# Kernel tuning notes

Hardware: AMD Instinct MI355X
Metric: run time of the kernel (lower is better)

The kernel has to match this reference:

```python
import jax, jax.numpy as jnp
import numpy as np

B, S, D = 1, 2048, 2048
H, HD = 16, 128  # n_heads, head_dim
ROPE_BASE = 100000.0


def setup_inputs() -> dict:
    key = jax.random.key(0)
    k0, k1, k2 = jax.random.split(key, 3)
    x = jax.random.normal(k0, (B, S, D), jnp.float32)
    # real RoPE table: (seq_len, head_dim//2, 2) holding (cos, sin)
    inv_freq = 1.0 / (ROPE_BASE ** (np.arange(0, HD, 2, dtype=np.float64) / HD))
    t = np.arange(S, dtype=np.float64)[:, None] * inv_freq[None, :]
    freqs_cis = jnp.asarray(np.stack([np.cos(t), np.sin(t)], axis=-1), jnp.float32)
    input_pos = jnp.arange(S, dtype=jnp.int32)
    Wqkv = jax.random.normal(k1, (D, 3 * D), jnp.float32) * (D ** -0.5)
    bqkv = jnp.zeros((3 * D,), jnp.float32)
    Wdense = jax.random.normal(k2, (D, D), jnp.float32) * (D ** -0.5)
    bdense = jnp.zeros((D,), jnp.float32)
    return {"x": x, "freqs_cis": freqs_cis, "input_pos": input_pos,
            "Wqkv": Wqkv, "bqkv": bqkv, "Wdense": Wdense, "bdense": bdense}


def apply_rotary_emb(x, freqs_cis):
    # x: [B, S, H, HD]; freqs_cis: [S, HD//2, 2]
    xs = x.reshape(*x.shape[:-1], -1, 2)  # [B,S,H,HD/2,2]
    fc = freqs_cis.reshape(1, xs.shape[1], 1, xs.shape[3], 2)
    out = jnp.stack([
        xs[..., 0] * fc[..., 0] - xs[..., 1] * fc[..., 1],
        xs[..., 1] * fc[..., 0] + xs[..., 0] * fc[..., 1],
    ], axis=-1)
    return out.reshape(x.shape).astype(x.dtype)


def reference(x, freqs_cis, input_pos, Wqkv, bqkv, Wdense, bdense):
    b, s, d = x.shape
    qkv = x @ Wqkv + bqkv                      # fused QKV projection
    q, k, v = jnp.split(qkv, 3, axis=-1)
    q = q.reshape(b, s, H, HD)
    k = k.reshape(b, s, H, HD)
    v = v.reshape(b, s, H, HD)
    q = apply_rotary_emb(q, freqs_cis)
    k = apply_rotary_emb(k, freqs_cis)
    # KV-cache update (cache batch = 1, max_seq = context_length)
    k_cache = jnp.zeros((1, S, H, HD), jnp.float32)
    v_cache = jnp.zeros((1, S, H, HD), jnp.float32)
    k_full = k_cache.at[:, input_pos].set(k)
    v_full = v_cache.at[:, input_pos].set(v)
    # causal SDPA in [B, H, S, HD] layout
    qh = q.transpose(0, 2, 1, 3)
    kh = k_full.transpose(0, 2, 1, 3)
    vh = v_full.transpose(0, 2, 1, 3)
    scale = HD ** -0.5
    scores = jnp.einsum('bhqd,bhkd->bhqk', qh, kh) * scale  # [B,H,S,S]
    causal = jnp.tril(jnp.ones((s, S), dtype=bool))
    scores = jnp.where(causal, scores, jnp.finfo(scores.dtype).min)
    attn = jax.nn.softmax(scores, axis=-1)
    ctx = jnp.einsum('bhqk,bhkd->bhqd', attn, vh)
    ctx = ctx.transpose(0, 2, 1, 3).reshape(b, s, d)
    return ctx @ Wdense + bdense
```

## Files before the change

kernel.cpp:

```cpp
#include <hip/hip_runtime.h>

#define S 2048
#define D 2048
#define H 16
#define HD 128
#define N3 6144

typedef __attribute__((ext_vector_type(8))) _Float16 f16x8;
typedef __attribute__((ext_vector_type(4))) float f32x4;
typedef unsigned short ushort_t;
typedef unsigned int uint_t;

__device__ __forceinline__ ushort_t f16_rne(float f) {
    _Float16 h = (_Float16)f;
    return __builtin_bit_cast(ushort_t, h);
}
__device__ __forceinline__ float f16_f32(ushort_t u) {
    return (float)__builtin_bit_cast(_Float16, u);
}

__global__ __launch_bounds__(256) void convert_f16_kernel(
    const float* __restrict__ in, ushort_t* __restrict__ hi)
{
    const int base = blockIdx.x * 512 + threadIdx.x;
    const float4* in4 = (const float4*)in;
    float4 a = in4[base];
    float4 b = in4[base + 256];
    ((ushort4*)hi)[base] = make_ushort4(f16_rne(a.x), f16_rne(a.y),
                                        f16_rne(a.z), f16_rne(a.w));
    ((ushort4*)hi)[base + 256] = make_ushort4(f16_rne(b.x), f16_rne(b.y),
                                              f16_rne(b.z), f16_rne(b.w));
}

__global__ __launch_bounds__(256) void convert_t_kernel(
    const float* __restrict__ in, ushort_t* __restrict__ hi,
    int Kdim, int Ndim)
{
    __shared__ float tile[32][33];
    const int k0 = blockIdx.x * 32, n0 = blockIdx.y * 32;
    const int row = threadIdx.x >> 3;
    const int c4  = (threadIdx.x & 7) * 4;
    float4 v = *(const float4*)&in[(size_t)(k0 + row) * Ndim + n0 + c4];
    tile[row][c4 + 0] = v.x;
    tile[row][c4 + 1] = v.y;
    tile[row][c4 + 2] = v.z;
    tile[row][c4 + 3] = v.w;
    __syncthreads();
    const int n  = threadIdx.x >> 3;
    const int kc = (threadIdx.x & 7) * 4;
    const float v0 = tile[kc + 0][n], v1 = tile[kc + 1][n];
    const float v2 = tile[kc + 2][n], v3 = tile[kc + 3][n];
    const size_t off = (size_t)(n0 + n) * Kdim + k0 + kc;
    *(ushort4*)&hi[off] = make_ushort4(f16_rne(v0), f16_rne(v1),
                                       f16_rne(v2), f16_rne(v3));
}

__device__ __forceinline__ void gload16(const ushort_t* g, ushort_t* l) {
    __builtin_amdgcn_global_load_lds(
        (const __attribute__((address_space(1))) unsigned int*)g,
        (__attribute__((address_space(3))) unsigned int*)l, 16, 0, 0);
}

__device__ __forceinline__ void vwait4() { asm volatile("s_waitcnt vmcnt(4)" ::: "memory"); }
__device__ __forceinline__ void vwait3() { asm volatile("s_waitcnt vmcnt(3)" ::: "memory"); }
__device__ __forceinline__ void vwait0() { asm volatile("s_waitcnt vmcnt(0)" ::: "memory"); }
__device__ __forceinline__ void lwait0() { asm volatile("s_waitcnt lgkmcnt(0)" ::: "memory"); }

#define QNT 32

__device__ __forceinline__ void mm_core_v4(
    const ushort_t* __restrict__ At, const ushort_t* __restrict__ Bt,
    ushort_t* lds, const int t, f32x4 (&acc)[4][2])
{
    const int w = t >> 6, lane = t & 63;
    const int lr = lane & 15, quad = lane >> 4;
    const int wm = (w >> 2) * 64;
    const int wn = (w & 3) * 32;

    const int srow = w * 8 + (lane >> 3);
    const int schk = ((lane & 7) ^ (lane >> 3)) * 8;
    const int ldsw = w * 512;

    auto stageAB = [&](int Tt) {
        ushort_t* dbase = lds + (Tt & 1) * 16384;
        const size_t koff = (size_t)Tt * 64 + schk;
        gload16(At + (size_t)srow * D + koff,        dbase + ldsw);
        gload16(At + (size_t)(srow + 64) * D + koff, dbase + 4096 + ldsw);
        gload16(Bt + (size_t)srow * D + koff,        dbase + 8192 + ldsw);
        gload16(Bt + (size_t)(srow + 64) * D + koff, dbase + 12288 + ldsw);
    };

    const int aoff = (wm + lr) * 64;
    const int boff = 8192 + (wn + lr) * 64;
    const int sw0 = ((0 * 4 + quad) ^ (lr & 7)) * 8;
    const int sw1 = ((1 * 4 + quad) ^ (lr & 7)) * 8;

    stageAB(0);
    stageAB(1);
    vwait4();
    __builtin_amdgcn_sched_barrier(0);
    __builtin_amdgcn_s_barrier();

    f16x8 a[4], b[2];
    for (int T = 0; T < QNT; T++) {
        const ushort_t* base = lds + (T & 1) * 16384;
        #pragma unroll
        for (int i = 0; i < 4; i++)
            a[i] = *(const f16x8*)&base[aoff + i * 1024 + sw0];
        #pragma unroll
        for (int n = 0; n < 2; n++)
            b[n] = *(const f16x8*)&base[boff + n * 1024 + sw0];
        lwait0();
        __builtin_amdgcn_sched_barrier(0);
        __builtin_amdgcn_s_setprio(1);
        #pragma unroll
        for (int i = 0; i < 4; i++)
            #pragma unroll
            for (int n = 0; n < 2; n++)
                acc[i][n] = __builtin_amdgcn_mfma_f32_16x16x32_f16(
                    a[i], b[n], acc[i][n], 0, 0, 0);
        __builtin_amdgcn_s_setprio(0);
        #pragma unroll
        for (int i = 0; i < 4; i++)
            a[i] = *(const f16x8*)&base[aoff + i * 1024 + sw1];
        #pragma unroll
        for (int n = 0; n < 2; n++)
            b[n] = *(const f16x8*)&base[boff + n * 1024 + sw1];
        lwait0();
        __builtin_amdgcn_sched_barrier(0);
        __builtin_amdgcn_s_barrier();
        if (T < QNT - 2) stageAB(T + 2);
        __builtin_amdgcn_s_setprio(1);
        #pragma unroll
        for (int i = 0; i < 4; i++)
            #pragma unroll
            for (int n = 0; n < 2; n++)
                acc[i][n] = __builtin_amdgcn_mfma_f32_16x16x32_f16(
                    a[i], b[n], acc[i][n], 0, 0, 0);
        __builtin_amdgcn_s_setprio(0);
        if (T < QNT - 2)       vwait4();
        else if (T == QNT - 2) vwait0();
        __builtin_amdgcn_s_barrier();
    }
}

__device__ __forceinline__ void mm_core_v4h(
    const ushort_t* __restrict__ At, const ushort_t* __restrict__ Bt,
    ushort_t* lds, const int t, f32x4 (&acc)[2][2])
{
    const int w = t >> 6, lane = t & 63;
    const int lr = lane & 15, quad = lane >> 4;
    const int wm = (w >> 2) * 32;
    const int wn = (w & 3) * 32;

    const int srow = w * 8 + (lane >> 3);
    const int schk = ((lane & 7) ^ (lane >> 3)) * 8;
    const int ldsw = w * 512;

    auto stageAB = [&](int Tt) {
        ushort_t* dbase = lds + (Tt & 1) * 12288;
        const size_t koff = (size_t)Tt * 64 + schk;
        gload16(At + (size_t)srow * D + koff,        dbase + ldsw);
        gload16(Bt + (size_t)srow * D + koff,        dbase + 4096 + ldsw);
        gload16(Bt + (size_t)(srow + 64) * D + koff, dbase + 8192 + ldsw);
    };

    const int aoff = (wm + lr) * 64;
    const int boff = 4096 + (wn + lr) * 64;
    const int sw0 = ((0 * 4 + quad) ^ (lr & 7)) * 8;
    const int sw1 = ((1 * 4 + quad) ^ (lr & 7)) * 8;

    stageAB(0);
    stageAB(1);
    vwait3();
    __builtin_amdgcn_sched_barrier(0);
    __builtin_amdgcn_s_barrier();

    f16x8 a[2], b[2];
    for (int T = 0; T < QNT; T++) {
        const ushort_t* base = lds + (T & 1) * 12288;
        #pragma unroll
        for (int i = 0; i < 2; i++)
            a[i] = *(const f16x8*)&base[aoff + i * 1024 + sw0];
        #pragma unroll
        for (int n = 0; n < 2; n++)
            b[n] = *(const f16x8*)&base[boff + n * 1024 + sw0];
        lwait0();
        __builtin_amdgcn_sched_barrier(0);
        __builtin_amdgcn_s_setprio(1);
        #pragma unroll
        for (int i = 0; i < 2; i++)
            #pragma unroll
            for (int n = 0; n < 2; n++)
                acc[i][n] = __builtin_amdgcn_mfma_f32_16x16x32_f16(
                    a[i], b[n], acc[i][n], 0, 0, 0);
        __builtin_amdgcn_s_setprio(0);
        #pragma unroll
        for (int i = 0; i < 2; i++)
            a[i] = *(const f16x8*)&base[aoff + i * 1024 + sw1];
        #pragma unroll
        for (int n = 0; n < 2; n++)
            b[n] = *(const f16x8*)&base[boff + n * 1024 + sw1];
        lwait0();
        __builtin_amdgcn_sched_barrier(0);
        __builtin_amdgcn_s_barrier();
        if (T < QNT - 2) stageAB(T + 2);
        __builtin_amdgcn_s_setprio(1);
        #pragma unroll
        for (int i = 0; i < 2; i++)
            #pragma unroll
            for (int n = 0; n < 2; n++)
                acc[i][n] = __builtin_amdgcn_mfma_f32_16x16x32_f16(
                    a[i], b[n], acc[i][n], 0, 0, 0);
        __builtin_amdgcn_s_setprio(0);
        if (T < QNT - 2)       vwait3();
        else if (T == QNT - 2) vwait0();
        __builtin_amdgcn_s_barrier();
    }
}

__global__ __launch_bounds__(512, 4) void gemm_qkv_mfma(
    const ushort_t* __restrict__ xh,
    const ushort_t* __restrict__ Wth,
    const float* __restrict__ bias, const float* __restrict__ freqs,
    const int* __restrict__ input_pos,
    ushort_t* __restrict__ qhg, ushort_t* __restrict__ khg,
    ushort_t* __restrict__ vhg)
{
    __shared__ ushort_t lds[32768];
    const int t = threadIdx.x;
    const int col0 = blockIdx.x * 128;
    const int row0 = blockIdx.y * 128;

    f32x4 acc[4][2] = {};
    mm_core_v4(xh + (size_t)row0 * D, Wth + (size_t)col0 * D, lds, t, acc);

    const int lane = t & 63;
    const int quad = lane >> 4;
    const int lr   = lane & 15;
    const int w = t >> 6;
    const int wm = (w >> 2) * 64;
    const int wn = (w & 3) * 32;

    const int which = col0 >> 11;
    const int hh = (col0 & 2047) >> 7;

    if (which == 2) {
        ushort_t* vh_b = vhg + (size_t)hh * HD * S;
        #pragma unroll
        for (int nt = 0; nt < 2; nt++) {
            const int d = wn + nt * 16 + lr;
            const float bsc = bias[col0 + d];
            #pragma unroll
            for (int mt = 0; mt < 4; mt++) {
                #pragma unroll
                for (int reg = 0; reg < 4; reg++) {
                    const int m = row0 + wm + mt * 16 + quad * 4 + reg;
                    const float v = acc[mt][nt][reg] + bsc;
                    vh_b[(size_t)d * S + input_pos[m]] = f16_rne(v);
                }
            }
        }
    } else {
        ushort_t* oh_b = ((which == 0) ? qhg : khg) + (size_t)hh * S * HD;
        #pragma unroll
        for (int nt = 0; nt < 2; nt++) {
            const int d = wn + nt * 16 + lr;
            const float bsc = bias[col0 + d];
            #pragma unroll
            for (int mt = 0; mt < 4; mt++) {
                #pragma unroll
                for (int reg = 0; reg < 4; reg++) {
                    const int m = row0 + wm + mt * 16 + quad * 4 + reg;
                    const float v = acc[mt][nt][reg] + bsc;
                    const float* fc = &freqs[((size_t)m * 64 + (d >> 1)) * 2];
                    const float cc = fc[0], ss = fc[1];
                    const float p = __shfl_xor(v, 1);
                    const float o = (d & 1) ? (v * cc + p * ss) : (v * cc - p * ss);
                    const ushort_t hv = f16_rne(o);
                    const int hp = __shfl_xor((int)hv, 1);
                    if (!(d & 1)) {
                        const int srowg = (which == 0) ? m : input_pos[m];
                        *(uint_t*)&oh_b[(size_t)srowg * HD + d] =
                            (uint_t)hv | ((uint_t)hp << 16);
                    }
                }
            }
        }
    }
}

__global__ __launch_bounds__(512, 4) void gemm_dense_mfma(
    const ushort_t* __restrict__ Ah,
    const ushort_t* __restrict__ Wth,
    const float* __restrict__ bias, float* __restrict__ out)
{
    __shared__ ushort_t lds[24576];
    const int t = threadIdx.x;
    const int col0 = blockIdx.x * 128;
    const int row0 = blockIdx.y * 64;

    f32x4 acc[2][2] = {};
    mm_core_v4h(Ah + (size_t)row0 * D, Wth + (size_t)col0 * D, lds, t, acc);

    const int lane = t & 63;
    const int quad = lane >> 4;
    const int lr   = lane & 15;
    const int w = t >> 6;
    const int wm = (w >> 2) * 32;
    const int wn = (w & 3) * 32;

    #pragma unroll
    for (int nt = 0; nt < 2; nt++) {
        const int n = col0 + wn + nt * 16 + lr;
        const float bsc = bias[n];
        #pragma unroll
        for (int mt = 0; mt < 2; mt++) {
            #pragma unroll
            for (int reg = 0; reg < 4; reg++) {
                const int m = row0 + wm + mt * 16 + quad * 4 + reg;
                const float o = acc[mt][nt][reg] + bsc;
                const float po = __shfl_xor(o, 1);
                if (!(n & 1))
                    *(float2*)&out[(size_t)m * D + n] = make_float2(o, po);
            }
        }
    }
}

__global__ __launch_bounds__(256, 4) void attn_mfma_kernel(
    const ushort_t* __restrict__ qhg, const ushort_t* __restrict__ khg,
    const ushort_t* __restrict__ vhg,
    float* __restrict__ Opart, float* __restrict__ MLpart)
{
    __shared__ ushort_t Khs[2][4096];
    __shared__ ushort_t Vhs[2][4096];
    __shared__ ushort_t Ps[64 * 32];

    const int bi   = blockIdx.x;
    const int h    = (bi & 7) + 8 * ((bi >> 3) & 1);
    const int half = (bi >> 4) & 1;
    const int qi   = bi >> 5;
    const int r = (h & 8) ? qi : (31 - qi);
    const int q0 = r * 64;
    const int nhalf = r + 1;
    const int kt0 = half * nhalf;
    const int kt1 = kt0 + nhalf;
    const int t = threadIdx.x;
    const int w = t >> 6, lane = t & 63;
    const int lr = lane & 15, quad = lane >> 4;

    const size_t qrow = (size_t)h * S + q0 + w * 16 + lr;
    f16x8 qf[4];
    #pragma unroll
    for (int ks = 0; ks < 4; ks++)
        qf[ks] = *(const f16x8*)&qhg[qrow * HD + ks * 32 + quad * 8];

    const ushort_t* kh_b = khg + (size_t)h * S * HD;
    const ushort_t* vh_b = vhg + (size_t)h * HD * S;

    const int keyq = lane >> 2;
    const int sub  = lane & 3;

    auto stage = [&](int kt, int buf) {
        const int k0 = kt * 32;
        #pragma unroll
        for (int hf = 0; hf < 2; hf++) {
            const size_t ksrc = (size_t)(k0 + hf * 16 + keyq) * HD + w * 32 + sub * 8;
            gload16(kh_b + ksrc, &Khs[buf][w * 1024 + hf * 512]);
            const int dim = w * 32 + hf * 16 + keyq;
            const size_t vsrc = (size_t)dim * S + k0 + sub * 8;
            gload16(vh_b + vsrc, &Vhs[buf][(w * 32 + hf * 16) * 32]);
        }
    };

    f32x4 O[8] = {};
    f32x4 Ol = {0.f, 0.f, 0.f, 0.f};
    float mrow[4];
    #pragma unroll
    for (int rr = 0; rr < 4; rr++) mrow[rr] = -1e30f;

    f16x8 onesv;
    #pragma unroll
    for (int i = 0; i < 8; i++) onesv[i] = (_Float16)1.0f;

    const float kSc = 0.08838834764831845f * 1.4426950408889634f;

    stage(kt0, 0);

    for (int kt = kt0; kt < kt1; kt++) {
        const int k0 = kt * 32;
        const int cur = (kt - kt0) & 1;
        __syncthreads();

        if (kt + 1 < kt1) stage(kt + 1, cur ^ 1);

        f32x4 sa[2];
        #pragma unroll
        for (int nt = 0; nt < 2; nt++) {
            f32x4 s = {0.f, 0.f, 0.f, 0.f};
            #pragma unroll
            for (int ks = 0; ks < 4; ks++) {
                f16x8 kf = *(const f16x8*)&Khs[cur][ks * 1024 + (nt * 16 + lr) * 32 + quad * 8];
                s = __builtin_amdgcn_mfma_f32_16x16x32_f16(qf[ks], kf, s, 0, 0, 0);
            }
            sa[nt] = s;
        }

        const int rowbase = q0 + w * 16 + quad * 4;
        const bool need_mask = (k0 + 31) > (q0 + w * 16);
        float alpha[4], pv0[4], pv1[4];
        #pragma unroll
        for (int rr = 0; rr < 4; rr++) {
            float z0 = sa[0][rr] * kSc;
            float z1 = sa[1][rr] * kSc;
            if (need_mask) {
                const int rowg = rowbase + rr;
                if (k0 + lr > rowg)      z0 = -1e30f;
                if (k0 + 16 + lr > rowg) z1 = -1e30f;
            }
            float rm = fmaxf(z0, z1);
            #pragma unroll
            for (int off = 1; off < 16; off <<= 1)
                rm = fmaxf(rm, __shfl_xor(rm, off));
            const float nm = fmaxf(mrow[rr], rm);
            alpha[rr] = exp2f(mrow[rr] - nm);
            pv0[rr] = exp2f(z0 - nm);
            pv1[rr] = exp2f(z1 - nm);
            mrow[rr] = nm;
        }

        #pragma unroll
        for (int rr = 0; rr < 4; rr++) {
            const int prow = (w * 16 + quad * 4 + rr) * 32;
            Ps[prow + lr]      = f16_rne(pv0[rr]);
            Ps[prow + 16 + lr] = f16_rne(pv1[rr]);
        }

        #pragma unroll
        for (int nt = 0; nt < 8; nt++)
            #pragma unroll
            for (int rr = 0; rr < 4; rr++)
                O[nt][rr] *= alpha[rr];
        #pragma unroll
        for (int rr = 0; rr < 4; rr++)
            Ol[rr] *= alpha[rr];
        const f16x8 pf = *(const f16x8*)&Ps[(w * 16 + lr) * 32 + quad * 8];
        #pragma unroll
        for (int nt = 0; nt < 8; nt++) {
            f16x8 vf = *(const f16x8*)&Vhs[cur][(nt * 16 + lr) * 32 + quad * 8];
            O[nt] = __builtin_amdgcn_mfma_f32_16x16x32_f16(pf, vf, O[nt], 0, 0, 0);
        }
        Ol = __builtin_amdgcn_mfma_f32_16x16x32_f16(pf, onesv, Ol, 0, 0, 0);
    }

    float* Ob = Opart + (size_t)bi * 64 * 128;
    #pragma unroll
    for (int rr = 0; rr < 4; rr++) {
        const int row = w * 16 + quad * 4 + rr;
        #pragma unroll
        for (int nt = 0; nt < 8; nt++)
            Ob[(size_t)row * 128 + nt * 16 + lr] = O[nt][rr];
        if (lr == 0) {
            MLpart[(size_t)bi * 128 + row * 2 + 0] = mrow[rr];
            MLpart[(size_t)bi * 128 + row * 2 + 1] = Ol[rr];
        }
    }
}

__global__ __launch_bounds__(128) void attn_combine_kernel(
    const float* __restrict__ Opart, const float* __restrict__ MLpart,
    ushort_t* __restrict__ ctxh)
{
    const int qt = blockIdx.x;
    const int h  = blockIdx.y;
    const int t  = threadIdx.x;
    const int b0 = h | (qt << 5);
    const int b1 = b0 | (1 << 4);
    const int r = (h & 8) ? qt : (31 - qt);
    const int q0 = r * 64;

    __shared__ float sc[64][2];
    if (t < 64) {
        const float m0 = MLpart[(size_t)b0 * 128 + t * 2 + 0];
        const float l0 = MLpart[(size_t)b0 * 128 + t * 2 + 1];
        const float m1 = MLpart[(size_t)b1 * 128 + t * 2 + 0];
        const float l1 = MLpart[(size_t)b1 * 128 + t * 2 + 1];
        const float m = fmaxf(m0, m1);
        const float a0 = exp2f(m0 - m), a1 = exp2f(m1 - m);
        const float inv = 1.0f / (l0 * a0 + l1 * a1);
        sc[t][0] = a0 * inv;
        sc[t][1] = a1 * inv;
    }
    __syncthreads();

    const float* O0 = Opart + (size_t)b0 * 64 * 128;
    const float* O1 = Opart + (size_t)b1 * 64 * 128;
    const int rb = t >> 5;
    const int c4 = (t & 31) * 4;
    for (int rs = 0; rs < 64; rs += 4) {
        const int row = rs + rb;
        float4 a = *(const float4*)&O0[(size_t)row * 128 + c4];
        float4 b = *(const float4*)&O1[(size_t)row * 128 + c4];
        const float s0 = sc[row][0], s1 = sc[row][1];
        ushort4 o = make_ushort4(f16_rne(a.x * s0 + b.x * s1),
                                 f16_rne(a.y * s0 + b.y * s1),
                                 f16_rne(a.z * s0 + b.z * s1),
                                 f16_rne(a.w * s0 + b.w * s1));
        *(ushort4*)&ctxh[(size_t)(q0 + row) * D + h * HD + c4] = o;
    }
}

__global__ __launch_bounds__(256) void gemm_qkv_kernel(
    const float* __restrict__ x, const float* __restrict__ W,
    const float* __restrict__ bias, const float* __restrict__ freqs,
    const int* __restrict__ input_pos,
    float* __restrict__ qb, float* __restrict__ kb, float* __restrict__ vb)
{
    __shared__ float As[16][68];
    __shared__ float Bs[16][64];
    const int bx = blockIdx.x;
    const int by = blockIdx.y;
    const int tid = threadIdx.x;
    const int tx = tid & 15, ty = tid >> 4;
    const int row0 = by * 64, col0 = bx * 64;
    const int am = tid >> 2;
    const int ak = (tid & 3) * 4;
    const int bk = tid >> 4;
    const int bn = (tid & 15) * 4;
    float acc[4][4] = {};
    for (int k0 = 0; k0 < D; k0 += 16) {
        float4 av = *(const float4*)&x[(size_t)(row0 + am) * D + k0 + ak];
        float4 bv = *(const float4*)&W[(size_t)(k0 + bk) * N3 + col0 + bn];
        __syncthreads();
        As[ak + 0][am] = av.x; As[ak + 1][am] = av.y;
        As[ak + 2][am] = av.z; As[ak + 3][am] = av.w;
        *(float4*)&Bs[bk][bn] = bv;
        __syncthreads();
        #pragma unroll
        for (int k = 0; k < 16; k++) {
            float4 a4 = *(const float4*)&As[k][ty * 4];
            float4 b4 = *(const float4*)&Bs[k][tx * 4];
            float a[4] = {a4.x, a4.y, a4.z, a4.w};
            float b[4] = {b4.x, b4.y, b4.z, b4.w};
            #pragma unroll
            for (int r = 0; r < 4; r++)
                #pragma unroll
                for (int c = 0; c < 4; c++)
                    acc[r][c] += a[r] * b[c];
        }
    }
    const int j0 = col0 + tx * 4;
    const int which = j0 >> 11;
    const int hh = (j0 & 2047) >> 7;
    const int d0 = j0 & 127;
    const float bv0 = bias[j0 + 0], bv1 = bias[j0 + 1];
    const float bv2 = bias[j0 + 2], bv3 = bias[j0 + 3];
    #pragma unroll
    for (int r = 0; r < 4; r++) {
        const int grow = row0 + ty * 4 + r;
        float v0 = acc[r][0] + bv0, v1 = acc[r][1] + bv1;
        float v2 = acc[r][2] + bv2, v3 = acc[r][3] + bv3;
        if (which == 2) {
            const int pos = input_pos[grow];
            float4 o4 = make_float4(v0, v1, v2, v3);
            *(float4*)&vb[((size_t)hh * S + pos) * HD + d0] = o4;
        } else {
            const float* fc = &freqs[((size_t)grow * 64 + (d0 >> 1)) * 2];
            float c0 = fc[0], s0 = fc[1], c1 = fc[2], s1 = fc[3];
            float o0 = v0 * c0 - v1 * s0, o1 = v1 * c0 + v0 * s0;
            float o2 = v2 * c1 - v3 * s1, o3 = v3 * c1 + v2 * s1;
            float4 o4 = make_float4(o0, o1, o2, o3);
            if (which == 0) {
                *(float4*)&qb[((size_t)hh * S + grow) * HD + d0] = o4;
            } else {
                const int pos = input_pos[grow];
                *(float4*)&kb[((size_t)hh * S + pos) * HD + d0] = o4;
            }
        }
    }
}

#define BQ 64
#define ABK 32
#define QSTR 132
#define KVSTR 132
#define PSTR 68

__global__ __launch_bounds__(256) void attn_kernel(
    const float* __restrict__ qb, const float* __restrict__ kb,
    const float* __restrict__ vb, float* __restrict__ ctx)
{
    __shared__ float Qs[BQ * QSTR];
    __shared__ float KV[ABK * KVSTR];
    __shared__ float Psf[ABK * PSTR];

    const int pa = blockIdx.x;
    const int h  = blockIdx.y;
    const int t  = threadIdx.x;
    const int ty = t >> 4, tx = t & 15;
    const int i0  = ty * 4;
    const int j0  = tx * 2;
    const int dd0 = tx * 8;
    const int lr = t >> 3;
    const int lc = (t & 7) * 4;

    const float* kbase = kb + (size_t)h * S * HD;
    const float* vbase = vb + (size_t)h * S * HD;
    const float kSc = 0.08838834764831845f * 1.4426950408889634f;

    for (int ph = 0; ph < 2; ph++) {
        const int r = (ph == 0) ? pa : 31 - pa;
        const int q0 = r * BQ;
        const int ntiles = 2 * r + 2;

        #pragma unroll
        for (int pp = 0; pp < 2; pp++) {
            const int iq = lr + pp * 32;
            const float* src = qb + ((size_t)h * S + q0 + iq) * HD;
            #pragma unroll
            for (int ch = 0; ch < 4; ch++)
                *(float4*)&Qs[iq * QSTR + lc + ch * 32] =
                    *(const float4*)&src[lc + ch * 32];
        }

        float O[4][8] = {};
        float m[4], l[4];
        #pragma unroll
        for (int rr = 0; rr < 4; rr++) { m[rr] = -1e30f; l[rr] = 0.f; }

        float4 kpref[4];
        #pragma unroll
        for (int ch = 0; ch < 4; ch++)
            kpref[ch] = *(const float4*)&kbase[(size_t)lr * HD + lc + ch * 32];

        __syncthreads();

        for (int kt = 0; kt < ntiles; kt++) {
            const int k0 = kt * ABK;

            #pragma unroll
            for (int ch = 0; ch < 4; ch++)
                *(float4*)&KV[lr * KVSTR + lc + ch * 32] = kpref[ch];
            __syncthreads();

            float4 vpref[4];
            #pragma unroll
            for (int ch = 0; ch < 4; ch++)
                vpref[ch] = *(const float4*)&vbase[(size_t)(k0 + lr) * HD + lc + ch * 32];

            float acc[4][2] = {};
            #pragma unroll 4
            for (int d0 = 0; d0 < HD; d0 += 4) {
                float4 ka = *(const float4*)&KV[(j0 + 0) * KVSTR + d0];
                float4 kb4 = *(const float4*)&KV[(j0 + 1) * KVSTR + d0];
                #pragma unroll
                for (int rr = 0; rr < 4; rr++) {
                    float4 q4 = *(const float4*)&Qs[(i0 + rr) * QSTR + d0];
                    acc[rr][0] += q4.x * ka.x + q4.y * ka.y + q4.z * ka.z + q4.w * ka.w;
                    acc[rr][1] += q4.x * kb4.x + q4.y * kb4.y + q4.z * kb4.z + q4.w * kb4.w;
                }
            }

            const bool need_mask = (k0 + ABK - 1) > q0;
            float p[4][2], alpha[4];
            #pragma unroll
            for (int rr = 0; rr < 4; rr++) {
                float z0 = acc[rr][0] * kSc;
                float z1 = acc[rr][1] * kSc;
                if (need_mask) {
                    if (k0 + j0 + 0 > q0 + i0 + rr) z0 = -1e30f;
                    if (k0 + j0 + 1 > q0 + i0 + rr) z1 = -1e30f;
                }
                float rmax = fmaxf(z0, z1);
                #pragma unroll
                for (int off = 1; off < 16; off <<= 1)
                    rmax = fmaxf(rmax, __shfl_xor(rmax, off, 16));
                const float nm = fmaxf(m[rr], rmax);
                alpha[rr] = exp2f(m[rr] - nm);
                p[rr][0] = exp2f(z0 - nm);
                p[rr][1] = exp2f(z1 - nm);
                float ts = p[rr][0] + p[rr][1];
                #pragma unroll
                for (int off = 1; off < 16; off <<= 1)
                    ts += __shfl_xor(ts, off, 16);
                l[rr] = l[rr] * alpha[rr] + ts;
                m[rr] = nm;
            }
            __syncthreads();

            #pragma unroll
            for (int ch = 0; ch < 4; ch++)
                *(float4*)&KV[lr * KVSTR + lc + ch * 32] = vpref[ch];
            *(float4*)&Psf[(j0 + 0) * PSTR + i0] =
                make_float4(p[0][0], p[1][0], p[2][0], p[3][0]);
            *(float4*)&Psf[(j0 + 1) * PSTR + i0] =
                make_float4(p[0][1], p[1][1], p[2][1], p[3][1]);
            if (kt + 1 < ntiles) {
                #pragma unroll
                for (int ch = 0; ch < 4; ch++)
                    kpref[ch] = *(const float4*)&kbase[(size_t)(k0 + ABK + lr) * HD + lc + ch * 32];
            }
            __syncthreads();

            #pragma unroll
            for (int rr = 0; rr < 4; rr++)
                #pragma unroll
                for (int c = 0; c < 8; c++)
                    O[rr][c] *= alpha[rr];
            #pragma unroll 4
            for (int j = 0; j < ABK; j++) {
                float4 pj = *(const float4*)&Psf[j * PSTR + i0];
                float4 v0 = *(const float4*)&KV[j * KVSTR + dd0];
                float4 v1 = *(const float4*)&KV[j * KVSTR + dd0 + 4];
                const float pr[4] = {pj.x, pj.y, pj.z, pj.w};
                const float vv[8] = {v0.x, v0.y, v0.z, v0.w, v1.x, v1.y, v1.z, v1.w};
                #pragma unroll
                for (int rr = 0; rr < 4; rr++)
                    #pragma unroll
                    for (int c = 0; c < 8; c++)
                        O[rr][c] += pr[rr] * vv[c];
            }
            __syncthreads();
        }

        #pragma unroll
        for (int rr = 0; rr < 4; rr++) {
            const float inv = 1.0f / l[rr];
            const int qg = q0 + i0 + rr;
            float4 o0 = make_float4(O[rr][0] * inv, O[rr][1] * inv,
                                    O[rr][2] * inv, O[rr][3] * inv);
            float4 o1 = make_float4(O[rr][4] * inv, O[rr][5] * inv,
                                    O[rr][6] * inv, O[rr][7] * inv);
            float* dst = &ctx[((size_t)qg * H + h) * HD + dd0];
            *(float4*)&dst[0] = o0;
            *(float4*)&dst[4] = o1;
        }
        __syncthreads();
    }
}

__global__ __launch_bounds__(256) void gemm_dense_kernel(
    const float* __restrict__ A, const float* __restrict__ W,
    const float* __restrict__ bias, float* __restrict__ out)
{
    __shared__ float As[16][68];
    __shared__ float Bs[16][64];
    const int bx = blockIdx.x;
    const int by = blockIdx.y;
    const int tid = threadIdx.x;
    const int tx = tid & 15, ty = tid >> 4;
    const int row0 = by * 64, col0 = bx * 64;
    const int am = tid >> 2;
    const int ak = (tid & 3) * 4;
    const int bk = tid >> 4;
    const int bn = (tid & 15) * 4;
    float acc[4][4] = {};
    for (int k0 = 0; k0 < D; k0 += 16) {
        float4 av = *(const float4*)&A[(size_t)(row0 + am) * D + k0 + ak];
        float4 bv = *(const float4*)&W[(size_t)(k0 + bk) * D + col0 + bn];
        __syncthreads();
        As[ak + 0][am] = av.x; As[ak + 1][am] = av.y;
        As[ak + 2][am] = av.z; As[ak + 3][am] = av.w;
        *(float4*)&Bs[bk][bn] = bv;
        __syncthreads();
        #pragma unroll
        for (int k = 0; k < 16; k++) {
            float4 a4 = *(const float4*)&As[k][ty * 4];
            float4 b4 = *(const float4*)&Bs[k][tx * 4];
            float a[4] = {a4.x, a4.y, a4.z, a4.w};
            float b[4] = {b4.x, b4.y, b4.z, b4.w};
            #pragma unroll
            for (int r = 0; r < 4; r++)
                #pragma unroll
                for (int c = 0; c < 4; c++)
                    acc[r][c] += a[r] * b[c];
        }
    }
    const int j0 = col0 + tx * 4;
    const float bv0 = bias[j0 + 0], bv1 = bias[j0 + 1];
    const float bv2 = bias[j0 + 2], bv3 = bias[j0 + 3];
    #pragma unroll
    for (int r = 0; r < 4; r++) {
        const int grow = row0 + ty * 4 + r;
        float4 o4 = make_float4(acc[r][0] + bv0, acc[r][1] + bv1,
                                acc[r][2] + bv2, acc[r][3] + bv3);
        *(float4*)&out[(size_t)grow * D + j0] = o4;
    }
}

extern "C" void kernel_launch(void* const* d_in, const int* in_sizes, int n_in,
                              void* d_out, int out_size, void* d_ws, size_t ws_size,
                              hipStream_t stream) {
    const float* x      = (const float*)d_in[0];
    const float* freqs  = (const float*)d_in[1];
    const int*   pos    = (const int*)d_in[2];
    const float* Wqkv   = (const float*)d_in[3];
    const float* bqkv   = (const float*)d_in[4];
    const float* Wdense = (const float*)d_in[5];
    const float* bdense = (const float*)d_in[6];
    float* out = (float*)d_out;

    const size_t nSD = (size_t)S * D;
    const size_t nW1 = (size_t)D * N3;
    const size_t nOP = (size_t)1024 * 64 * 128;
    const size_t nML = (size_t)1024 * 128;

    const size_t needed =
        (6 * nSD + nW1) * sizeof(ushort_t) + (nOP + nML) * sizeof(float);

    if (ws_size >= needed) {
        ushort_t* qh   = (ushort_t*)d_ws;
        ushort_t* kh   = qh + nSD;
        ushort_t* vh   = kh + nSD;
        ushort_t* ctxh = vh + nSD;
        ushort_t* xh   = ctxh + nSD;
        ushort_t* Wth  = xh + nSD;
        ushort_t* Wdth = Wth + nW1;
        float* Opart = (float*)(Wdth + nSD);
        float* MLpart = Opart + nOP;

        convert_f16_kernel<<<nSD / 4 / 512, 256, 0, stream>>>(x, xh);
        dim3 gt1(D / 32, N3 / 32);
        convert_t_kernel<<<gt1, 256, 0, stream>>>(Wqkv, Wth, D, N3);
        dim3 gt2(D / 32, D / 32);
        convert_t_kernel<<<gt2, 256, 0, stream>>>(Wdense, Wdth, D, D);

        dim3 g1(N3 / 128, S / 128);
        gemm_qkv_mfma<<<g1, 512, 0, stream>>>(xh, Wth, bqkv, freqs,
                                              pos, qh, kh, vh);
        attn_mfma_kernel<<<1024, 256, 0, stream>>>(qh, kh, vh,
                                                   Opart, MLpart);
        dim3 gc(32, H);
        attn_combine_kernel<<<gc, 128, 0, stream>>>(Opart, MLpart, ctxh);
        dim3 g3(D / 128, S / 64);
        gemm_dense_mfma<<<g3, 512, 0, stream>>>(ctxh, Wdth, bdense, out);
    } else {
        float* qb  = (float*)d_ws;
        float* kb  = qb + (size_t)H * S * HD;
        float* vb  = kb + (size_t)H * S * HD;
        float* ctx = vb + (size_t)H * S * HD;
        dim3 g1(N3 / 64, S / 64);
        gemm_qkv_kernel<<<g1, 256, 0, stream>>>(x, Wqkv, bqkv, freqs, pos, qb, kb, vb);
        dim3 g2(16, H);
        attn_kernel<<<g2, 256, 0, stream>>>(qb, kb, vb, ctx);
        dim3 g3(D / 64, S / 64);
        gemm_dense_kernel<<<g3, 256, 0, stream>>>(ctx, Wdense, bdense, out);
    }
}
```

Baseline: 315.5 us.

## Widen QKV GEMM tile to 192 columns and store attention partials in fp16

The QKV projection GEMM tile is widened from 128x128 to 128x192. Each wave now computes a 64x48 sub-tile with a third B fragment, which raises arithmetic intensity per LDS stage and cuts the grid to 512 blocks. The epilogue now derives head, section and offset per column, since a tile can now span multiple heads. Separately, the split-K attention partial outputs are normalized and stored as fp16 instead of fp32, and the combine kernel's weights are reworked to match. This halves partial-output traffic at some precision cost, while the larger tile uses more registers and LDS, which may reduce occupancy.

```diff
diff --git a/kernel.cpp b/kernel.cpp
--- a/kernel.cpp
+++ b/kernel.cpp
@@ -61,33 +61,36 @@
         (__attribute__((address_space(3))) unsigned int*)l, 16, 0, 0);
 }
 
-__device__ __forceinline__ void vwait4() { asm volatile("s_waitcnt vmcnt(4)" ::: "memory"); }
+__device__ __forceinline__ void vwait5() { asm volatile("s_waitcnt vmcnt(5)" ::: "memory"); }
 __device__ __forceinline__ void vwait3() { asm volatile("s_waitcnt vmcnt(3)" ::: "memory"); }
 __device__ __forceinline__ void vwait0() { asm volatile("s_waitcnt vmcnt(0)" ::: "memory"); }
 __device__ __forceinline__ void lwait0() { asm volatile("s_waitcnt lgkmcnt(0)" ::: "memory"); }
 
 #define QNT 32
 
-__device__ __forceinline__ void mm_core_v4(
+#define BUFW 20480
+
+__device__ __forceinline__ void mm_core_v4w(
     const ushort_t* __restrict__ At, const ushort_t* __restrict__ Bt,
-    ushort_t* lds, const int t, f32x4 (&acc)[4][2])
+    ushort_t* lds, const int t, f32x4 (&acc)[4][3])
 {
     const int w = t >> 6, lane = t & 63;
     const int lr = lane & 15, quad = lane >> 4;
     const int wm = (w >> 2) * 64;
-    const int wn = (w & 3) * 32;
+    const int wn = (w & 3) * 48;
 
     const int srow = w * 8 + (lane >> 3);
     const int schk = ((lane & 7) ^ (lane >> 3)) * 8;
     const int ldsw = w * 512;
 
     auto stageAB = [&](int Tt) {
-        ushort_t* dbase = lds + (Tt & 1) * 16384;
+        ushort_t* dbase = lds + (Tt & 1) * BUFW;
         const size_t koff = (size_t)Tt * 64 + schk;
-        gload16(At + (size_t)srow * D + koff,        dbase + ldsw);
-        gload16(At + (size_t)(srow + 64) * D + koff, dbase + 4096 + ldsw);
-        gload16(Bt + (size_t)srow * D + koff,        dbase + 8192 + ldsw);
-        gload16(Bt + (size_t)(srow + 64) * D + koff, dbase + 12288 + ldsw);
+        gload16(At + (size_t)srow * D + koff,         dbase + ldsw);
+        gload16(At + (size_t)(srow + 64) * D + koff,  dbase + 4096 + ldsw);
+        gload16(Bt + (size_t)srow * D + koff,         dbase + 8192 + ldsw);
+        gload16(Bt + (size_t)(srow + 64) * D + koff,  dbase + 12288 + ldsw);
+        gload16(Bt + (size_t)(srow + 128) * D + koff, dbase + 16384 + ldsw);
     };
 
     const int aoff = (wm + lr) * 64;
@@ -97,15 +100,90 @@
 
     stageAB(0);
     stageAB(1);
-    vwait4();
+    vwait5();
     __builtin_amdgcn_sched_barrier(0);
     __builtin_amdgcn_s_barrier();
 
-    f16x8 a[4], b[2];
+    f16x8 a[4], b[3];
     for (int T = 0; T < QNT; T++) {
-        const ushort_t* base = lds + (T & 1) * 16384;
+        const ushort_t* base = lds + (T & 1) * BUFW;
         #pragma unroll
         for (int i = 0; i < 4; i++)
+            a[i] = *(const f16x8*)&base[aoff + i * 1024 + sw0];
+        #pragma unroll
+        for (int n = 0; n < 3; n++)
+            b[n] = *(const f16x8*)&base[boff + n * 1024 + sw0];
+        lwait0();
+        __builtin_amdgcn_sched_barrier(0);
+        __builtin_amdgcn_s_setprio(1);
+        #pragma unroll
+        for (int i = 0; i < 4; i++)
+            #pragma unroll
+            for (int n = 0; n < 3; n++)
+                acc[i][n] = __builtin_amdgcn_mfma_f32_16x16x32_f16(
+                    a[i], b[n], acc[i][n], 0, 0, 0);
+        __builtin_amdgcn_s_setprio(0);
+        #pragma unroll
+        for (int i = 0; i < 4; i++)
+            a[i] = *(const f16x8*)&base[aoff + i * 1024 + sw1];
+        #pragma unroll
+        for (int n = 0; n < 3; n++)
+            b[n] = *(const f16x8*)&base[boff + n * 1024 + sw1];
+        lwait0();
+        __builtin_amdgcn_sched_barrier(0);
+        __builtin_amdgcn_s_barrier();
+        if (T < QNT - 2) stageAB(T + 2);
+        __builtin_amdgcn_s_setprio(1);
+        #pragma unroll
+        for (int i = 0; i < 4; i++)
+            #pragma unroll
+            for (int n = 0; n < 3; n++)
+                acc[i][n] = __builtin_amdgcn_mfma_f32_16x16x32_f16(
+                    a[i], b[n], acc[i][n], 0, 0, 0);
+        __builtin_amdgcn_s_setprio(0);
+        if (T < QNT - 2)       vwait5();
+        else if (T == QNT - 2) vwait0();
+        __builtin_amdgcn_s_barrier();
+    }
+}
+
+__device__ __forceinline__ void mm_core_v4h(
+    const ushort_t* __restrict__ At, const ushort_t* __restrict__ Bt,
+    ushort_t* lds, const int t, f32x4 (&acc)[2][2])
+{
+    const int w = t >> 6, lane = t & 63;
+    const int lr = lane & 15, quad = lane >> 4;
+    const int wm = (w >> 2) * 32;
+    const int wn = (w & 3) * 32;
+
+    const int srow = w * 8 + (lane >> 3);
+    const int schk = ((lane & 7) ^ (lane >> 3)) * 8;
+    const int ldsw = w * 512;
+
+    auto stageAB = [&](int Tt) {
+        ushort_t* dbase = lds + (Tt & 1) * 12288;
+        const size_t koff = (size_t)Tt * 64 + schk;
+        gload16(At + (size_t)srow * D + koff,        dbase + ldsw);
+        gload16(Bt + (size_t)srow * D + koff,        dbase + 4096 + ldsw);
+        gload16(Bt + (size_t)(srow + 64) * D + koff, dbase + 8192 + ldsw);
+    };
+
+    const int aoff = (wm + lr) * 64;
+    const int boff = 4096 + (wn + lr) * 64;
+    const int sw0 = ((0 * 4 + quad) ^ (lr & 7)) * 8;
+    const int sw1 = ((1 * 4 + quad) ^ (lr & 7)) * 8;
+
+    stageAB(0);
+    stageAB(1);
+    vwait3();
+    __builtin_amdgcn_sched_barrier(0);
+    __builtin_amdgcn_s_barrier();
+
+    f16x8 a[2], b[2];
+    for (int T = 0; T < QNT; T++) {
+        const ushort_t* base = lds + (T & 1) * 12288;
+        #pragma unroll
+        for (int i = 0; i < 2; i++)
             a[i] = *(const f16x8*)&base[aoff + i * 1024 + sw0];
         #pragma unroll
         for (int n = 0; n < 2; n++)
@@ -114,14 +192,14 @@
         __builtin_amdgcn_sched_barrier(0);
         __builtin_amdgcn_s_setprio(1);
         #pragma unroll
-        for (int i = 0; i < 4; i++)
+        for (int i = 0; i < 2; i++)
             #pragma unroll
             for (int n = 0; n < 2; n++)
                 acc[i][n] = __builtin_amdgcn_mfma_f32_16x16x32_f16(
                     a[i], b[n], acc[i][n], 0, 0, 0);
         __builtin_amdgcn_s_setprio(0);
         #pragma unroll
-        for (int i = 0; i < 4; i++)
+        for (int i = 0; i < 2; i++)
             a[i] = *(const f16x8*)&base[aoff + i * 1024 + sw1];
         #pragma unroll
         for (int n = 0; n < 2; n++)
@@ -132,81 +210,6 @@
         if (T < QNT - 2) stageAB(T + 2);
         __builtin_amdgcn_s_setprio(1);
         #pragma unroll
-        for (int i = 0; i < 4; i++)
-            #pragma unroll
-            for (int n = 0; n < 2; n++)
-                acc[i][n] = __builtin_amdgcn_mfma_f32_16x16x32_f16(
-                    a[i], b[n], acc[i][n], 0, 0, 0);
-        __builtin_amdgcn_s_setprio(0);
-        if (T < QNT - 2)       vwait4();
-        else if (T == QNT - 2) vwait0();
-        __builtin_amdgcn_s_barrier();
-    }
-}
-
-__device__ __forceinline__ void mm_core_v4h(
-    const ushort_t* __restrict__ At, const ushort_t* __restrict__ Bt,
-    ushort_t* lds, const int t, f32x4 (&acc)[2][2])
-{
-    const int w = t >> 6, lane = t & 63;
-    const int lr = lane & 15, quad = lane >> 4;
-    const int wm = (w >> 2) * 32;
-    const int wn = (w & 3) * 32;
-
-    const int srow = w * 8 + (lane >> 3);
-    const int schk = ((lane & 7) ^ (lane >> 3)) * 8;
-    const int ldsw = w * 512;
-
-    auto stageAB = [&](int Tt) {
-        ushort_t* dbase = lds + (Tt & 1) * 12288;
-        const size_t koff = (size_t)Tt * 64 + schk;
-        gload16(At + (size_t)srow * D + koff,        dbase + ldsw);
-        gload16(Bt + (size_t)srow * D + koff,        dbase + 4096 + ldsw);
-        gload16(Bt + (size_t)(srow + 64) * D + koff, dbase + 8192 + ldsw);
-    };
-
-    const int aoff = (wm + lr) * 64;
-    const int boff = 4096 + (wn + lr) * 64;
-    const int sw0 = ((0 * 4 + quad) ^ (lr & 7)) * 8;
-    const int sw1 = ((1 * 4 + quad) ^ (lr & 7)) * 8;
-
-    stageAB(0);
-    stageAB(1);
-    vwait3();
-    __builtin_amdgcn_sched_barrier(0);
-    __builtin_amdgcn_s_barrier();
-
-    f16x8 a[2], b[2];
-    for (int T = 0; T < QNT; T++) {
-        const ushort_t* base = lds + (T & 1) * 12288;
-        #pragma unroll
-        for (int i = 0; i < 2; i++)
-            a[i] = *(const f16x8*)&base[aoff + i * 1024 + sw0];
-        #pragma unroll
-        for (int n = 0; n < 2; n++)
-            b[n] = *(const f16x8*)&base[boff + n * 1024 + sw0];
-        lwait0();
-        __builtin_amdgcn_sched_barrier(0);
-        __builtin_amdgcn_s_setprio(1);
-        #pragma unroll
-        for (int i = 0; i < 2; i++)
-            #pragma unroll
-            for (int n = 0; n < 2; n++)
-                acc[i][n] = __builtin_amdgcn_mfma_f32_16x16x32_f16(
-                    a[i], b[n], acc[i][n], 0, 0, 0);
-        __builtin_amdgcn_s_setprio(0);
-        #pragma unroll
-        for (int i = 0; i < 2; i++)
-            a[i] = *(const f16x8*)&base[aoff + i * 1024 + sw1];
-        #pragma unroll
-        for (int n = 0; n < 2; n++)
-            b[n] = *(const f16x8*)&base[boff + n * 1024 + sw1];
-        lwait0();
-        __builtin_amdgcn_sched_barrier(0);
-        __builtin_amdgcn_s_barrier();
-        if (T < QNT - 2) stageAB(T + 2);
-        __builtin_amdgcn_s_setprio(1);
-        #pragma unroll
         for (int i = 0; i < 2; i++)
             #pragma unroll
             for (int n = 0; n < 2; n++)
@@ -227,30 +230,30 @@
     ushort_t* __restrict__ qhg, ushort_t* __restrict__ khg,
     ushort_t* __restrict__ vhg)
 {
-    __shared__ ushort_t lds[32768];
+    __shared__ ushort_t lds[2 * BUFW];
     const int t = threadIdx.x;
-    const int col0 = blockIdx.x * 128;
+    const int col0 = blockIdx.x * 192;
     const int row0 = blockIdx.y * 128;
 
-    f32x4 acc[4][2] = {};
-    mm_core_v4(xh + (size_t)row0 * D, Wth + (size_t)col0 * D, lds, t, acc);
+    f32x4 acc[4][3] = {};
+    mm_core_v4w(xh + (size_t)row0 * D, Wth + (size_t)col0 * D, lds, t, acc);
 
     const int lane = t & 63;
     const int quad = lane >> 4;
     const int lr   = lane & 15;
     const int w = t >> 6;
     const int wm = (w >> 2) * 64;
-    const int wn = (w & 3) * 32;
-
-    const int which = col0 >> 11;
-    const int hh = (col0 & 2047) >> 7;
-
-    if (which == 2) {
-        ushort_t* vh_b = vhg + (size_t)hh * HD * S;
-        #pragma unroll
-        for (int nt = 0; nt < 2; nt++) {
-            const int d = wn + nt * 16 + lr;
-            const float bsc = bias[col0 + d];
+    const int wn = (w & 3) * 48;
+
+    #pragma unroll
+    for (int nt = 0; nt < 3; nt++) {
+        const int c = col0 + wn + nt * 16 + lr;
+        const int which = c >> 11;
+        const int hh = (c & 2047) >> 7;
+        const int d = c & 127;
+        const float bsc = bias[c];
+        if (which == 2) {
+            ushort_t* vh_b = vhg + (size_t)hh * HD * S;
             #pragma unroll
             for (int mt = 0; mt < 4; mt++) {
                 #pragma unroll
@@ -260,13 +263,8 @@
                     vh_b[(size_t)d * S + input_pos[m]] = f16_rne(v);
                 }
             }
-        }
-    } else {
-        ushort_t* oh_b = ((which == 0) ? qhg : khg) + (size_t)hh * S * HD;
-        #pragma unroll
-        for (int nt = 0; nt < 2; nt++) {
-            const int d = wn + nt * 16 + lr;
-            const float bsc = bias[col0 + d];
+        } else {
+            ushort_t* oh_b = ((which == 0) ? qhg : khg) + (size_t)hh * S * HD;
             #pragma unroll
             for (int mt = 0; mt < 4; mt++) {
                 #pragma unroll
@@ -331,7 +329,7 @@
 __global__ __launch_bounds__(256, 4) void attn_mfma_kernel(
     const ushort_t* __restrict__ qhg, const ushort_t* __restrict__ khg,
     const ushort_t* __restrict__ vhg,
-    float* __restrict__ Opart, float* __restrict__ MLpart)
+    ushort_t* __restrict__ Opart, float* __restrict__ MLpart)
 {
     __shared__ ushort_t Khs[2][4096];
     __shared__ ushort_t Vhs[2][4096];
@@ -454,13 +452,14 @@
         Ol = __builtin_amdgcn_mfma_f32_16x16x32_f16(pf, onesv, Ol, 0, 0, 0);
     }
 
-    float* Ob = Opart + (size_t)bi * 64 * 128;
+    ushort_t* Ob = Opart + (size_t)bi * 64 * 128;
     #pragma unroll
     for (int rr = 0; rr < 4; rr++) {
         const int row = w * 16 + quad * 4 + rr;
+        const float inv = (Ol[rr] > 0.f) ? 1.0f / Ol[rr] : 0.f;
         #pragma unroll
         for (int nt = 0; nt < 8; nt++)
-            Ob[(size_t)row * 128 + nt * 16 + lr] = O[nt][rr];
+            Ob[(size_t)row * 128 + nt * 16 + lr] = f16_rne(O[nt][rr] * inv);
         if (lr == 0) {
             MLpart[(size_t)bi * 128 + row * 2 + 0] = mrow[rr];
             MLpart[(size_t)bi * 128 + row * 2 + 1] = Ol[rr];
@@ -469,7 +468,7 @@
 }
 
 __global__ __launch_bounds__(128) void attn_combine_kernel(
-    const float* __restrict__ Opart, const float* __restrict__ MLpart,
+    const ushort_t* __restrict__ Opart, const float* __restrict__ MLpart,
     ushort_t* __restrict__ ctxh)
 {
     const int qt = blockIdx.x;
@@ -487,26 +486,28 @@
         const float m1 = MLpart[(size_t)b1 * 128 + t * 2 + 0];
         const float l1 = MLpart[(size_t)b1 * 128 + t * 2 + 1];
         const float m = fmaxf(m0, m1);
-        const float a0 = exp2f(m0 - m), a1 = exp2f(m1 - m);
-        const float inv = 1.0f / (l0 * a0 + l1 * a1);
-        sc[t][0] = a0 * inv;
-        sc[t][1] = a1 * inv;
+        const float w0 = exp2f(m0 - m) * l0;
+        const float w1 = exp2f(m1 - m) * l1;
+        const float inv = 1.0f / (w0 + w1);
+        sc[t][0] = w0 * inv;
+        sc[t][1] = w1 * inv;
     }
     __syncthreads();
 
-    const float* O0 = Opart + (size_t)b0 * 64 * 128;
-    const float* O1 = Opart + (size_t)b1 * 64 * 128;
+    const ushort_t* O0 = Opart + (size_t)b0 * 64 * 128;
+    const ushort_t* O1 = Opart + (size_t)b1 * 64 * 128;
     const int rb = t >> 5;
     const int c4 = (t & 31) * 4;
     for (int rs = 0; rs < 64; rs += 4) {
         const int row = rs + rb;
-        float4 a = *(const float4*)&O0[(size_t)row * 128 + c4];
-        float4 b = *(const float4*)&O1[(size_t)row * 128 + c4];
+        ushort4 ua = *(const ushort4*)&O0[(size_t)row * 128 + c4];
+        ushort4 ub = *(const ushort4*)&O1[(size_t)row * 128 + c4];
         const float s0 = sc[row][0], s1 = sc[row][1];
-        ushort4 o = make_ushort4(f16_rne(a.x * s0 + b.x * s1),
-                                 f16_rne(a.y * s0 + b.y * s1),
-                                 f16_rne(a.z * s0 + b.z * s1),
-                                 f16_rne(a.w * s0 + b.w * s1));
+        ushort4 o = make_ushort4(
+            f16_rne(f16_f32(ua.x) * s0 + f16_f32(ub.x) * s1),
+            f16_rne(f16_f32(ua.y) * s0 + f16_f32(ub.y) * s1),
+            f16_rne(f16_f32(ua.z) * s0 + f16_f32(ub.z) * s1),
+            f16_rne(f16_f32(ua.w) * s0 + f16_f32(ub.w) * s1));
         *(ushort4*)&ctxh[(size_t)(q0 + row) * D + h * HD + c4] = o;
     }
 }
@@ -807,7 +808,7 @@
     const size_t nML = (size_t)1024 * 128;
 
     const size_t needed =
-        (6 * nSD + nW1) * sizeof(ushort_t) + (nOP + nML) * sizeof(float);
+        (6 * nSD + nW1 + nOP) * sizeof(ushort_t) + nML * sizeof(float);
 
     if (ws_size >= needed) {
         ushort_t* qh   = (ushort_t*)d_ws;
@@ -817,8 +818,8 @@
         ushort_t* xh   = ctxh + nSD;
         ushort_t* Wth  = xh + nSD;
         ushort_t* Wdth = Wth + nW1;
-        float* Opart = (float*)(Wdth + nSD);
-        float* MLpart = Opart + nOP;
+        ushort_t* Opart = Wdth + nSD;
+        float* MLpart = (float*)(Opart + nOP);
 
         convert_f16_kernel<<<nSD / 4 / 512, 256, 0, stream>>>(x, xh);
         dim3 gt1(D / 32, N3 / 32);
@@ -826,7 +827,7 @@
         dim3 gt2(D / 32, D / 32);
         convert_t_kernel<<<gt2, 256, 0, stream>>>(Wdense, Wdth, D, D);
 
-        dim3 g1(N3 / 128, S / 128);
+        dim3 g1(N3 / 192, S / 128);
         gemm_qkv_mfma<<<g1, 512, 0, stream>>>(xh, Wth, bqkv, freqs,
                                               pos, qh, kh, vh);
         attn_mfma_kernel<<<1024, 256, 0, stream>>>(qh, kh, vh,
```

Measured after the change: 300.3 us (median of 2 runs). -4.8%, faster.
